# Kernel tuning notes

Measured on AMD Instinct MI355X. Metric: run time of the kernel, lower is better.

## Reference

```python
import jax, jax.numpy as jnp
import numpy as np

NEG_BIG = jnp.finfo(jnp.float32).min  # torch.nan_to_num maps -inf to finfo.min


def setup_inputs() -> dict:
    key = jax.random.key(0)
    ks = jax.random.split(key, 6)
    B, S, IN_KQ, IN_V, OUT_KQ, OUT_V = 4, 4096, 512, 512, 64, 64
    query = jax.random.normal(ks[0], (B, S, IN_KQ), dtype=jnp.float32)
    key_t = jax.random.normal(ks[1], (B, S, IN_KQ), dtype=jnp.float32)
    value = jax.random.normal(ks[2], (B, S, IN_V), dtype=jnp.float32)
    # nn.Linear weights: shape [out, in], y = x @ W.T
    Wq = jax.random.normal(ks[3], (OUT_KQ, IN_KQ), dtype=jnp.float32) / np.sqrt(IN_KQ)
    Wk = jax.random.normal(ks[4], (OUT_KQ, IN_KQ), dtype=jnp.float32) / np.sqrt(IN_KQ)
    Wv = jax.random.normal(ks[5], (OUT_V, IN_V), dtype=jnp.float32) / np.sqrt(IN_V)
    return {"query": query, "key": key_t, "value": value, "Wq": Wq, "Wk": Wk, "Wv": Wv}


def reference(query, key, value, Wq, Wk, Wv):
    # QKV projections (Linear, no bias): [B,S,in] @ [in,out]
    Q = jnp.einsum('bsi,oi->bso', query, Wq)
    K = jnp.einsum('bsi,oi->bso', key, Wk)
    V = jnp.einsum('bsi,oi->bso', value, Wv)

    S = Q.shape[1]
    scale = Q.shape[-1] ** 0.5
    # temp[b,i,j] = Q_i . K_j
    temp = jnp.einsum('bid,bjd->bij', Q, K)
    # torch mask: triu (incl. diagonal) -> finfo.min, strictly lower -> 0
    upper = jnp.triu(jnp.ones((S, S), dtype=bool), k=0)
    mask = jnp.where(upper, NEG_BIG, 0.0).astype(temp.dtype)
    # scale applied AFTER adding mask, as in the source
    attention = jax.nn.softmax((temp + mask) / scale, axis=-1)
    out = jnp.einsum('bij,bjd->bid', attention, V)
    return out
```

## Files before the change

### kernel.cpp

```cpp
#include <hip/hip_runtime.h>
#include <stdint.h>

#define Bn  4
#define Sn  4096
#define DIN 512
#define Dn  64
#define RS  0.18033688011112042f
#define MASKV (-3.0e38f)

typedef __bf16 bf16;
typedef __bf16 bf16x8 __attribute__((ext_vector_type(8)));
typedef float  f32x16 __attribute__((ext_vector_type(16)));
typedef unsigned short ushort8_t __attribute__((ext_vector_type(8)));

__device__ __forceinline__ f32x16 mfma32(bf16x8 a, bf16x8 b, f32x16 c) {
  return __builtin_amdgcn_mfma_f32_32x32x16_bf16(a, b, c, 0, 0, 0);
}

__device__ __forceinline__ f32x16 fzero16() {
  f32x16 v;
#pragma unroll
  for (int i = 0; i < 16; ++i) v[i] = 0.f;
  return v;
}

__device__ __forceinline__ bf16x8 frag_ld(const unsigned short* base, int row, int k) {
  int off = (row << 7) + (k << 1);
  off ^= (row & 7) << 4;
  return *(const bf16x8*)((const char*)base + off);
}

__device__ __forceinline__ void async16(void* lds, const void* g) {
  __builtin_amdgcn_global_load_lds(
      (const __attribute__((address_space(1))) unsigned int*)g,
      (__attribute__((address_space(3))) unsigned int*)lds, 16, 0, 0);
}

__device__ __forceinline__ unsigned int pk2(float a, float b) {
  unsigned short ra = __builtin_bit_cast(unsigned short, (bf16)a);
  unsigned short rb = __builtin_bit_cast(unsigned short, (bf16)b);
  return (unsigned int)ra | ((unsigned int)rb << 16);
}

__global__ __launch_bounds__(256) void proj_kernel(
    const float* __restrict__ Xq, const float* __restrict__ Xk, const float* __restrict__ Xv,
    const float* __restrict__ Wq, const float* __restrict__ Wk, const float* __restrict__ Wv,
    unsigned short* __restrict__ Qh, unsigned short* __restrict__ Ql,
    unsigned short* __restrict__ Kh, unsigned short* __restrict__ Kl,
    unsigned short* __restrict__ Vh, unsigned short* __restrict__ Vl)
{
  int mat = blockIdx.x >> 8;
  int rt  = blockIdx.x & 255;
  const float* X = (mat == 0) ? Xq : (mat == 1) ? Xk : Xv;
  const float* W = (mat == 0) ? Wq : (mat == 1) ? Wk : Wv;
  unsigned short* Yh = (mat == 0) ? Qh : (mat == 1) ? Kh : Vh;
  unsigned short* Yl = (mat == 0) ? Ql : (mat == 1) ? Kl : Vl;

  __shared__ unsigned short Xh_s[64 * 64];
  __shared__ unsigned short Xl_s[64 * 64];
  __shared__ unsigned short Wh_s[64 * 64];
  __shared__ unsigned short Wl_s[64 * 64];

  int tid  = threadIdx.x;
  int lane = tid & 63;
  int wv   = tid >> 6;
  int h    = lane >> 5;
  int c    = lane & 31;
  int srow = tid >> 2;
  int sq   = tid & 3;

  int row0 = rt * 64;

  f32x16 acc = fzero16();

  for (int k0 = 0; k0 < DIN; k0 += 64) {
#pragma unroll
    for (int j = 0; j < 4; ++j) {
      int kk = j * 16 + sq * 4;
      int off = ((srow << 7) + (kk << 1)) ^ ((srow & 7) << 4);

      float4 xv = *(const float4*)(X + (size_t)(row0 + srow) * DIN + k0 + kk);
      bf16 bx0 = (bf16)xv.x, bx1 = (bf16)xv.y, bx2 = (bf16)xv.z, bx3 = (bf16)xv.w;
      uint2 hw, lw;
      hw.x = (unsigned)__builtin_bit_cast(unsigned short, bx0) |
             ((unsigned)__builtin_bit_cast(unsigned short, bx1) << 16);
      hw.y = (unsigned)__builtin_bit_cast(unsigned short, bx2) |
             ((unsigned)__builtin_bit_cast(unsigned short, bx3) << 16);
      lw.x = pk2(xv.x - (float)bx0, xv.y - (float)bx1);
      lw.y = pk2(xv.z - (float)bx2, xv.w - (float)bx3);
      *(uint2*)((char*)Xh_s + off) = hw;
      *(uint2*)((char*)Xl_s + off) = lw;

      float4 wv4 = *(const float4*)(W + (size_t)srow * DIN + k0 + kk);
      bf16 bw0 = (bf16)wv4.x, bw1 = (bf16)wv4.y, bw2 = (bf16)wv4.z, bw3 = (bf16)wv4.w;
      uint2 hw2, lw2;
      hw2.x = (unsigned)__builtin_bit_cast(unsigned short, bw0) |
              ((unsigned)__builtin_bit_cast(unsigned short, bw1) << 16);
      hw2.y = (unsigned)__builtin_bit_cast(unsigned short, bw2) |
              ((unsigned)__builtin_bit_cast(unsigned short, bw3) << 16);
      lw2.x = pk2(wv4.x - (float)bw0, wv4.y - (float)bw1);
      lw2.y = pk2(wv4.z - (float)bw2, wv4.w - (float)bw3);
      *(uint2*)((char*)Wh_s + off) = hw2;
      *(uint2*)((char*)Wl_s + off) = lw2;
    }
    __syncthreads();

    int ar   = (wv >> 1) * 32 + c;
    int bcol = (wv & 1) * 32 + c;
#pragma unroll
    for (int kk = 0; kk < 4; ++kk) {
      int kp = kk * 16 + h * 8;
      bf16x8 ah = frag_ld(Xh_s, ar, kp);
      bf16x8 al = frag_ld(Xl_s, ar, kp);
      bf16x8 bh = frag_ld(Wh_s, bcol, kp);
      bf16x8 bl = frag_ld(Wl_s, bcol, kp);
      acc = mfma32(ah, bh, acc);
      acc = mfma32(ah, bl, acc);
      acc = mfma32(al, bh, acc);
    }
    __syncthreads();
  }

  int wr = (wv >> 1) * 32;
  int wc = (wv & 1) * 32;
#pragma unroll
  for (int r = 0; r < 16; ++r) {
    int rowl = (r & 3) + ((r >> 2) << 3) + h * 4;
    size_t o = (size_t)(row0 + wr + rowl) * Dn + wc + c;
    float v = acc[r];
    bf16 hv = (bf16)v;
    Yh[o] = __builtin_bit_cast(unsigned short, hv);
    Yl[o] = __builtin_bit_cast(unsigned short, (bf16)(v - (float)hv));
  }
}

__global__ __launch_bounds__(256) void transpose_kernel(
    const unsigned short* __restrict__ Vh, const unsigned short* __restrict__ Vl,
    unsigned short* __restrict__ Vth, unsigned short* __restrict__ Vtl)
{
  int bx = blockIdx.x;
  int b  = bx >> 6;
  int s0 = (bx & 63) * 64;
  __shared__ unsigned short th[64][72];
  __shared__ unsigned short tl[64][72];
  int t = threadIdx.x;
  int r = t >> 2, q4 = t & 3;

  const unsigned short* srch = Vh + ((size_t)(b * Sn + s0 + r)) * Dn + q4 * 16;
  const unsigned short* srcl = Vl + ((size_t)(b * Sn + s0 + r)) * Dn + q4 * 16;
  ushort8_t a0 = *(const ushort8_t*)srch;
  ushort8_t a1 = *(const ushort8_t*)(srch + 8);
  ushort8_t b0 = *(const ushort8_t*)srcl;
  ushort8_t b1 = *(const ushort8_t*)(srcl + 8);
  *(ushort8_t*)&th[r][q4 * 16]     = a0;
  *(ushort8_t*)&th[r][q4 * 16 + 8] = a1;
  *(ushort8_t*)&tl[r][q4 * 16]     = b0;
  *(ushort8_t*)&tl[r][q4 * 16 + 8] = b1;
  __syncthreads();

  int d = t >> 2, sp = t & 3;
  ushort8_t o0, o1, p0, p1;
#pragma unroll
  for (int i = 0; i < 8; ++i) {
    o0[i] = th[sp * 16 + i][d];
    o1[i] = th[sp * 16 + 8 + i][d];
    p0[i] = tl[sp * 16 + i][d];
    p1[i] = tl[sp * 16 + 8 + i][d];
  }
  unsigned short* dsth = Vth + ((size_t)(b * Dn + d)) * Sn + s0 + sp * 16;
  unsigned short* dstl = Vtl + ((size_t)(b * Dn + d)) * Sn + s0 + sp * 16;
  *(ushort8_t*)dsth       = o0;
  *(ushort8_t*)(dsth + 8) = o1;
  *(ushort8_t*)dstl       = p0;
  *(ushort8_t*)(dstl + 8) = p1;
}

__global__ __launch_bounds__(128) void attn_kernel(
    const unsigned short* __restrict__ Qh, const unsigned short* __restrict__ Ql,
    const unsigned short* __restrict__ Kh, const unsigned short* __restrict__ Kl,
    const unsigned short* __restrict__ Vth, const unsigned short* __restrict__ Vtl,
    float* __restrict__ part)
{
  int bx   = blockIdx.x;
  int qt   = 63 - (bx >> 3);
  int half = (bx >> 2) & 1;
  int b    = bx & 3;
  int tid  = threadIdx.x;
  int wv   = tid >> 6;
  int lane = tid & 63;
  int h    = lane >> 5;
  int c    = lane & 31;
  int q_base = qt * 64 + wv * 32;

  __shared__ unsigned short Kh_s[2][64 * 64];
  __shared__ unsigned short Kl_s[2][64 * 64];
  __shared__ unsigned short Vh_s[2][64 * 64];
  __shared__ unsigned short Vl_s[2][64 * 64];

  bf16x8 qhi[4], qlo[4];
  {
    const unsigned short* qp  = Qh + ((size_t)(b * Sn) + q_base + c) * Dn;
    const unsigned short* qp2 = Ql + ((size_t)(b * Sn) + q_base + c) * Dn;
#pragma unroll
    for (int kk = 0; kk < 4; ++kk) {
      qhi[kk] = *(const bf16x8*)(qp + kk * 16 + h * 8);
      qlo[kk] = *(const bf16x8*)(qp2 + kk * 16 + h * 8);
    }
  }

  f32x16 o0 = fzero16(), o1 = fzero16();
  float m = MASKV, lsum = 0.f;
  int nt = qt + 1;

  int l8   = lane >> 3;
  int slot = (lane & 7) ^ (l8 & 7);

  auto stage = [&](int sb, int ti) {
    size_t j0 = (size_t)ti * 64;
#pragma unroll
    for (int i = 0; i < 4; ++i) {
      int rowbase = (wv * 4 + i) * 8;
      int row = rowbase + l8;
      const char* gk  = (const char*)Kh + ((size_t)(b * Sn) + j0 + row) * 128 + slot * 16;
      const char* gk2 = (const char*)Kl + ((size_t)(b * Sn) + j0 + row) * 128 + slot * 16;
      async16(&Kh_s[sb][rowbase * 64], gk);
      async16(&Kl_s[sb][rowbase * 64], gk2);
      const char* gv  = (const char*)Vth + ((size_t)(b * Dn) + row) * (Sn * 2) + j0 * 2 + slot * 16;
      const char* gv2 = (const char*)Vtl + ((size_t)(b * Dn) + row) * (Sn * 2) + j0 * 2 + slot * 16;
      async16(&Vh_s[sb][rowbase * 64], gv);
      async16(&Vl_s[sb][rowbase * 64], gv2);
    }
  };

  int buf = 0;
  stage(0, half);
  __syncthreads();

  for (int ti = half; ti < nt; ti += 2) {
    if (ti + 2 < nt) stage(buf ^ 1, ti + 2);

    const unsigned short* KhT = Kh_s[buf];
    const unsigned short* KlT = Kl_s[buf];
    const unsigned short* VhT = Vh_s[buf];
    const unsigned short* VlT = Vl_s[buf];

    f32x16 s0a = fzero16(), s0b = fzero16(), s1a = fzero16(), s1b = fzero16();
#pragma unroll
    for (int kk = 0; kk < 4; ++kk) {
      int kp = kk * 16 + h * 8;
      bf16x8 k0h = frag_ld(KhT, c, kp);
      bf16x8 k0l = frag_ld(KlT, c, kp);
      bf16x8 k1h = frag_ld(KhT, 32 + c, kp);
      bf16x8 k1l = frag_ld(KlT, 32 + c, kp);
      if (kk < 2) {
        s0a = mfma32(k0h, qhi[kk], s0a); s0a = mfma32(k0h, qlo[kk], s0a); s0a = mfma32(k0l, qhi[kk], s0a);
        s1a = mfma32(k1h, qhi[kk], s1a); s1a = mfma32(k1h, qlo[kk], s1a); s1a = mfma32(k1l, qhi[kk], s1a);
      } else {
        s0b = mfma32(k0h, qhi[kk], s0b); s0b = mfma32(k0h, qlo[kk], s0b); s0b = mfma32(k0l, qhi[kk], s0b);
        s1b = mfma32(k1h, qhi[kk], s1b); s1b = mfma32(k1h, qlo[kk], s1b); s1b = mfma32(k1l, qhi[kk], s1b);
      }
    }
    f32x16 s0 = s0a + s0b;
    f32x16 s1 = s1a + s1b;

    if (ti == qt) {
      int qrel = wv * 32 + c;
#pragma unroll
      for (int r = 0; r < 16; ++r) {
        int koff = (r & 3) + ((r >> 2) << 3) + h * 4;
        if (koff >= qrel)      s0[r] = MASKV;
        if (32 + koff >= qrel) s1[r] = MASKV;
      }
    }

    float mt = s0[0];
#pragma unroll
    for (int r = 1; r < 16; ++r) mt = fmaxf(mt, s0[r]);
#pragma unroll
    for (int r = 0; r < 16; ++r) mt = fmaxf(mt, s1[r]);
    mt = fmaxf(mt, __shfl_xor(mt, 32, 64));
    float mnew = fmaxf(m, mt);
    float al = exp2f((m - mnew) * RS);

    float p0[16], p1[16];
    float rsum = 0.f;
#pragma unroll
    for (int r = 0; r < 16; ++r) {
      p0[r] = exp2f((s0[r] - mnew) * RS);
      p1[r] = exp2f((s1[r] - mnew) * RS);
      rsum += p0[r] + p1[r];
    }
    rsum += __shfl_xor(rsum, 32, 64);
    lsum = lsum * al + rsum;
    m = mnew;

#pragma unroll
    for (int r = 0; r < 16; ++r) {
      int koff = (r & 3) + ((r >> 2) << 3) + h * 4;
      float ar = __shfl(al, (lane & 32) | koff, 64);
      o0[r] *= ar;
      o1[r] *= ar;
    }

#pragma unroll
    for (int ks = 0; ks < 2; ++ks) {
#pragma unroll
      for (int kk2 = 0; kk2 < 2; ++kk2) {
        float e0[4], e1[4];
#pragma unroll
        for (int x = 0; x < 4; ++x) {
          float vh0 = ks ? p1[(2 * kk2 + 0) * 4 + x] : p0[(2 * kk2 + 0) * 4 + x];
          float vh1 = ks ? p1[(2 * kk2 + 1) * 4 + x] : p0[(2 * kk2 + 1) * 4 + x];
          float own  = h ? vh1 : vh0;
          float send = h ? vh0 : vh1;
          float recv = __shfl_xor(send, 32, 64);
          e0[x] = h ? recv : own;
          e1[x] = h ? own : recv;
        }
        bf16x8 pah, pal;
#pragma unroll
        for (int x = 0; x < 4; ++x) {
          bf16 hh = (bf16)e0[x];
          pah[x] = hh;
          pal[x] = (bf16)(e0[x] - (float)hh);
          bf16 h2 = (bf16)e1[x];
          pah[4 + x] = h2;
          pal[4 + x] = (bf16)(e1[x] - (float)h2);
        }
        int kp = ks * 32 + kk2 * 16 + h * 8;
        bf16x8 v0h = frag_ld(VhT, c, kp);
        bf16x8 v0l = frag_ld(VlT, c, kp);
        bf16x8 v1h = frag_ld(VhT, 32 + c, kp);
        bf16x8 v1l = frag_ld(VlT, 32 + c, kp);
        o0 = mfma32(pah, v0h, o0);
        o0 = mfma32(pah, v0l, o0);
        o0 = mfma32(pal, v0h, o0);
        o1 = mfma32(pah, v1h, o1);
        o1 = mfma32(pah, v1l, o1);
        o1 = mfma32(pal, v1h, o1);
      }
    }

    __syncthreads();
    buf ^= 1;
  }

  float* pb = part + ((size_t)(half * Bn + b) * Sn + q_base) * 68;
#pragma unroll
  for (int r = 0; r < 16; ++r) {
    int koff = (r & 3) + ((r >> 2) << 3) + h * 4;
    float* pr = pb + (size_t)koff * 68;
    pr[c]      = o0[r];
    pr[32 + c] = o1[r];
  }
  if (h == 0) {
    float* pr = pb + (size_t)c * 68;
    pr[64] = m;
    pr[65] = lsum;
  }
}

__global__ __launch_bounds__(256) void combine_kernel(
    const float* __restrict__ part, float* __restrict__ out)
{
  size_t idx = (size_t)blockIdx.x * 256 + threadIdx.x;
  int d = (int)(idx & 63);
  int s = (int)((idx >> 6) & (Sn - 1));
  int b = (int)(idx >> 18);
  const float* p0 = part + ((size_t)(0 * Bn + b) * Sn + s) * 68;
  const float* p1 = part + ((size_t)(1 * Bn + b) * Sn + s) * 68;
  float m0 = p0[64], l0 = p0[65];
  float m1 = p1[64], l1 = p1[65];
  float ms = fmaxf(m0, m1);
  float a0 = exp2f((m0 - ms) * RS);
  float a1 = exp2f((m1 - ms) * RS);
  float num = a0 * p0[d] + a1 * p1[d];
  float den = a0 * l0 + a1 * l1;
  out[idx] = (s == 0) ? 0.0f : (num / den);
}

__global__ __launch_bounds__(256) void meanv_kernel(
    const unsigned short* __restrict__ Vth, const unsigned short* __restrict__ Vtl,
    float* __restrict__ out)
{
  int bx = blockIdx.x;
  int b  = bx >> 4;
  int dg = (bx & 15) * 4;
  int t  = threadIdx.x;
  int dl = t >> 6;
  int jl = t & 63;
  int d  = dg + dl;

  const unsigned short* ph = Vth + ((size_t)(b * Dn + d)) * Sn;
  const unsigned short* pl = Vtl + ((size_t)(b * Dn + d)) * Sn;
  float s = 0.f;
#pragma unroll
  for (int it = 0; it < 4; ++it) {
    int base = it * 1024 + jl * 16;
    ushort8_t v0 = *(const ushort8_t*)(ph + base);
    ushort8_t v1 = *(const ushort8_t*)(ph + base + 8);
    ushort8_t w0 = *(const ushort8_t*)(pl + base);
    ushort8_t w1 = *(const ushort8_t*)(pl + base + 8);
#pragma unroll
    for (int e = 0; e < 8; ++e) {
      s += __uint_as_float((unsigned)v0[e] << 16);
      s += __uint_as_float((unsigned)v1[e] << 16);
      s += __uint_as_float((unsigned)w0[e] << 16);
      s += __uint_as_float((unsigned)w1[e] << 16);
    }
  }
#pragma unroll
  for (int o = 32; o > 0; o >>= 1) s += __shfl_xor(s, o, 64);
  if (jl == 0) out[(size_t)b * Sn * Dn + d] = s * (1.0f / 4096.0f);
}

extern "C" void kernel_launch(void* const* d_in, const int* in_sizes, int n_in,
                              void* d_out, int out_size, void* d_ws, size_t ws_size,
                              hipStream_t stream) {
  (void)in_sizes; (void)n_in; (void)out_size; (void)ws_size;
  const float* query = (const float*)d_in[0];
  const float* key_  = (const float*)d_in[1];
  const float* value = (const float*)d_in[2];
  const float* Wq = (const float*)d_in[3];
  const float* Wk = (const float*)d_in[4];
  const float* Wv = (const float*)d_in[5];
  float* out = (float*)d_out;

  char* w = (char*)d_ws;
  const size_t mat = (size_t)Bn * Sn * Dn * 2;
  unsigned short* Qh  = (unsigned short*)(w + 0 * mat);
  unsigned short* Ql  = (unsigned short*)(w + 1 * mat);
  unsigned short* Kh  = (unsigned short*)(w + 2 * mat);
  unsigned short* Kl  = (unsigned short*)(w + 3 * mat);
  unsigned short* Vh  = (unsigned short*)(w + 4 * mat);
  unsigned short* Vl  = (unsigned short*)(w + 5 * mat);
  unsigned short* Vth = (unsigned short*)(w + 6 * mat);
  unsigned short* Vtl = (unsigned short*)(w + 7 * mat);
  float* part = (float*)(w + 8 * mat);

  hipLaunchKernelGGL(proj_kernel, dim3(768), dim3(256), 0, stream,
                     query, key_, value, Wq, Wk, Wv, Qh, Ql, Kh, Kl, Vh, Vl);
  hipLaunchKernelGGL(transpose_kernel, dim3(256), dim3(256), 0, stream,
                     Vh, Vl, Vth, Vtl);
  hipLaunchKernelGGL(attn_kernel, dim3(512), dim3(128), 0, stream,
                     Qh, Ql, Kh, Kl, Vth, Vtl, part);
  hipLaunchKernelGGL(combine_kernel, dim3((Bn * Sn * Dn) / 256), dim3(256), 0, stream,
                     part, out);
  hipLaunchKernelGGL(meanv_kernel, dim3(64), dim3(256), 0, stream,
                     Vth, Vtl, out);
}
```

Measured before the change: 253.9 us.

## Fuse V transpose into projection and split attention KV four ways with 128-row query tiles

The projection kernel now writes V directly in transposed layout, which removes the separate transpose kernel and its extra round trip through memory. The attention kernel switches to 256-thread blocks covering 128 query rows each and splits the KV range four ways instead of two. Each staged K/V tile is shared by four waves, and waves skip tiles past their own diagonal. The combine kernel merges four partial results. In exchange, the transposed V stores from the projection are strided, some waves sit idle on diagonal tiles, and the partial buffer roughly doubles in size.

```diff
diff --git a/kernel.cpp b/kernel.cpp
--- a/kernel.cpp
+++ b/kernel.cpp
@@ -47,14 +47,14 @@
     const float* __restrict__ Wq, const float* __restrict__ Wk, const float* __restrict__ Wv,
     unsigned short* __restrict__ Qh, unsigned short* __restrict__ Ql,
     unsigned short* __restrict__ Kh, unsigned short* __restrict__ Kl,
-    unsigned short* __restrict__ Vh, unsigned short* __restrict__ Vl)
+    unsigned short* __restrict__ Vth, unsigned short* __restrict__ Vtl)
 {
   int mat = blockIdx.x >> 8;
   int rt  = blockIdx.x & 255;
   const float* X = (mat == 0) ? Xq : (mat == 1) ? Xk : Xv;
   const float* W = (mat == 0) ? Wq : (mat == 1) ? Wk : Wv;
-  unsigned short* Yh = (mat == 0) ? Qh : (mat == 1) ? Kh : Vh;
-  unsigned short* Yl = (mat == 0) ? Ql : (mat == 1) ? Kl : Vl;
+  unsigned short* Yh = (mat == 0) ? Qh : (mat == 1) ? Kh : Vth;
+  unsigned short* Yl = (mat == 0) ? Ql : (mat == 1) ? Kl : Vtl;
 
   __shared__ unsigned short Xh_s[64 * 64];
   __shared__ unsigned short Xl_s[64 * 64];
@@ -123,74 +123,48 @@
 
   int wr = (wv >> 1) * 32;
   int wc = (wv & 1) * 32;
-#pragma unroll
-  for (int r = 0; r < 16; ++r) {
-    int rowl = (r & 3) + ((r >> 2) << 3) + h * 4;
-    size_t o = (size_t)(row0 + wr + rowl) * Dn + wc + c;
-    float v = acc[r];
-    bf16 hv = (bf16)v;
-    Yh[o] = __builtin_bit_cast(unsigned short, hv);
-    Yl[o] = __builtin_bit_cast(unsigned short, (bf16)(v - (float)hv));
-  }
-}
-
-__global__ __launch_bounds__(256) void transpose_kernel(
-    const unsigned short* __restrict__ Vh, const unsigned short* __restrict__ Vl,
-    unsigned short* __restrict__ Vth, unsigned short* __restrict__ Vtl)
-{
-  int bx = blockIdx.x;
-  int b  = bx >> 6;
-  int s0 = (bx & 63) * 64;
-  __shared__ unsigned short th[64][72];
-  __shared__ unsigned short tl[64][72];
-  int t = threadIdx.x;
-  int r = t >> 2, q4 = t & 3;
-
-  const unsigned short* srch = Vh + ((size_t)(b * Sn + s0 + r)) * Dn + q4 * 16;
-  const unsigned short* srcl = Vl + ((size_t)(b * Sn + s0 + r)) * Dn + q4 * 16;
-  ushort8_t a0 = *(const ushort8_t*)srch;
-  ushort8_t a1 = *(const ushort8_t*)(srch + 8);
-  ushort8_t b0 = *(const ushort8_t*)srcl;
-  ushort8_t b1 = *(const ushort8_t*)(srcl + 8);
-  *(ushort8_t*)&th[r][q4 * 16]     = a0;
-  *(ushort8_t*)&th[r][q4 * 16 + 8] = a1;
-  *(ushort8_t*)&tl[r][q4 * 16]     = b0;
-  *(ushort8_t*)&tl[r][q4 * 16 + 8] = b1;
-  __syncthreads();
-
-  int d = t >> 2, sp = t & 3;
-  ushort8_t o0, o1, p0, p1;
-#pragma unroll
-  for (int i = 0; i < 8; ++i) {
-    o0[i] = th[sp * 16 + i][d];
-    o1[i] = th[sp * 16 + 8 + i][d];
-    p0[i] = tl[sp * 16 + i][d];
-    p1[i] = tl[sp * 16 + 8 + i][d];
-  }
-  unsigned short* dsth = Vth + ((size_t)(b * Dn + d)) * Sn + s0 + sp * 16;
-  unsigned short* dstl = Vtl + ((size_t)(b * Dn + d)) * Sn + s0 + sp * 16;
-  *(ushort8_t*)dsth       = o0;
-  *(ushort8_t*)(dsth + 8) = o1;
-  *(ushort8_t*)dstl       = p0;
-  *(ushort8_t*)(dstl + 8) = p1;
-}
-
-__global__ __launch_bounds__(128) void attn_kernel(
+  if (mat == 2) {
+#pragma unroll
+    for (int r = 0; r < 16; ++r) {
+      int rowl = (r & 3) + ((r >> 2) << 3) + h * 4;
+      int g  = row0 + wr + rowl;
+      int b2 = g >> 12;
+      int s2 = g & (Sn - 1);
+      size_t o = ((size_t)(b2 * Dn + wc + c)) * Sn + s2;
+      float v = acc[r];
+      bf16 hv = (bf16)v;
+      Yh[o] = __builtin_bit_cast(unsigned short, hv);
+      Yl[o] = __builtin_bit_cast(unsigned short, (bf16)(v - (float)hv));
+    }
+  } else {
+#pragma unroll
+    for (int r = 0; r < 16; ++r) {
+      int rowl = (r & 3) + ((r >> 2) << 3) + h * 4;
+      size_t o = (size_t)(row0 + wr + rowl) * Dn + wc + c;
+      float v = acc[r];
+      bf16 hv = (bf16)v;
+      Yh[o] = __builtin_bit_cast(unsigned short, hv);
+      Yl[o] = __builtin_bit_cast(unsigned short, (bf16)(v - (float)hv));
+    }
+  }
+}
+
+__global__ __launch_bounds__(256) void attn_kernel(
     const unsigned short* __restrict__ Qh, const unsigned short* __restrict__ Ql,
     const unsigned short* __restrict__ Kh, const unsigned short* __restrict__ Kl,
     const unsigned short* __restrict__ Vth, const unsigned short* __restrict__ Vtl,
     float* __restrict__ part)
 {
   int bx   = blockIdx.x;
-  int qt   = 63 - (bx >> 3);
-  int half = (bx >> 2) & 1;
+  int qtb  = 31 - (bx >> 4);
+  int sk   = (bx >> 2) & 3;
   int b    = bx & 3;
   int tid  = threadIdx.x;
   int wv   = tid >> 6;
   int lane = tid & 63;
   int h    = lane >> 5;
   int c    = lane & 31;
-  int q_base = qt * 64 + wv * 32;
+  int q_base = qtb * 128 + wv * 32;
 
   __shared__ unsigned short Kh_s[2][64 * 64];
   __shared__ unsigned short Kl_s[2][64 * 64];
@@ -210,7 +184,10 @@
 
   f32x16 o0 = fzero16(), o1 = fzero16();
   float m = MASKV, lsum = 0.f;
-  int nt = qt + 1;
+
+  int nt   = 2 * qtb + 2;
+  int ti_d = 2 * qtb + (wv >> 1);
+  int qrel = (wv & 1) * 32 + c;
 
   int l8   = lane >> 3;
   int slot = (lane & 7) ^ (l8 & 7);
@@ -218,8 +195,8 @@
   auto stage = [&](int sb, int ti) {
     size_t j0 = (size_t)ti * 64;
 #pragma unroll
-    for (int i = 0; i < 4; ++i) {
-      int rowbase = (wv * 4 + i) * 8;
+    for (int i = 0; i < 2; ++i) {
+      int rowbase = (wv * 2 + i) * 8;
       int row = rowbase + l8;
       const char* gk  = (const char*)Kh + ((size_t)(b * Sn) + j0 + row) * 128 + slot * 16;
       const char* gk2 = (const char*)Kl + ((size_t)(b * Sn) + j0 + row) * 128 + slot * 16;
@@ -233,111 +210,113 @@
   };
 
   int buf = 0;
-  stage(0, half);
+  stage(0, sk);
   __syncthreads();
 
-  for (int ti = half; ti < nt; ti += 2) {
-    if (ti + 2 < nt) stage(buf ^ 1, ti + 2);
-
-    const unsigned short* KhT = Kh_s[buf];
-    const unsigned short* KlT = Kl_s[buf];
-    const unsigned short* VhT = Vh_s[buf];
-    const unsigned short* VlT = Vl_s[buf];
-
-    f32x16 s0a = fzero16(), s0b = fzero16(), s1a = fzero16(), s1b = fzero16();
-#pragma unroll
-    for (int kk = 0; kk < 4; ++kk) {
-      int kp = kk * 16 + h * 8;
-      bf16x8 k0h = frag_ld(KhT, c, kp);
-      bf16x8 k0l = frag_ld(KlT, c, kp);
-      bf16x8 k1h = frag_ld(KhT, 32 + c, kp);
-      bf16x8 k1l = frag_ld(KlT, 32 + c, kp);
-      if (kk < 2) {
-        s0a = mfma32(k0h, qhi[kk], s0a); s0a = mfma32(k0h, qlo[kk], s0a); s0a = mfma32(k0l, qhi[kk], s0a);
-        s1a = mfma32(k1h, qhi[kk], s1a); s1a = mfma32(k1h, qlo[kk], s1a); s1a = mfma32(k1l, qhi[kk], s1a);
-      } else {
-        s0b = mfma32(k0h, qhi[kk], s0b); s0b = mfma32(k0h, qlo[kk], s0b); s0b = mfma32(k0l, qhi[kk], s0b);
-        s1b = mfma32(k1h, qhi[kk], s1b); s1b = mfma32(k1h, qlo[kk], s1b); s1b = mfma32(k1l, qhi[kk], s1b);
+  for (int ti = sk; ti < nt; ti += 4) {
+    if (ti + 4 < nt) stage(buf ^ 1, ti + 4);
+
+    bool active = (ti <= ti_d);
+    if (active) {
+      const unsigned short* KhT = Kh_s[buf];
+      const unsigned short* KlT = Kl_s[buf];
+      const unsigned short* VhT = Vh_s[buf];
+      const unsigned short* VlT = Vl_s[buf];
+
+      f32x16 s0a = fzero16(), s0b = fzero16(), s1a = fzero16(), s1b = fzero16();
+#pragma unroll
+      for (int kk = 0; kk < 4; ++kk) {
+        int kp = kk * 16 + h * 8;
+        bf16x8 k0h = frag_ld(KhT, c, kp);
+        bf16x8 k0l = frag_ld(KlT, c, kp);
+        bf16x8 k1h = frag_ld(KhT, 32 + c, kp);
+        bf16x8 k1l = frag_ld(KlT, 32 + c, kp);
+        if (kk < 2) {
+          s0a = mfma32(k0h, qhi[kk], s0a); s0a = mfma32(k0h, qlo[kk], s0a); s0a = mfma32(k0l, qhi[kk], s0a);
+          s1a = mfma32(k1h, qhi[kk], s1a); s1a = mfma32(k1h, qlo[kk], s1a); s1a = mfma32(k1l, qhi[kk], s1a);
+        } else {
+          s0b = mfma32(k0h, qhi[kk], s0b); s0b = mfma32(k0h, qlo[kk], s0b); s0b = mfma32(k0l, qhi[kk], s0b);
+          s1b = mfma32(k1h, qhi[kk], s1b); s1b = mfma32(k1h, qlo[kk], s1b); s1b = mfma32(k1l, qhi[kk], s1b);
+        }
       }
-    }
-    f32x16 s0 = s0a + s0b;
-    f32x16 s1 = s1a + s1b;
-
-    if (ti == qt) {
-      int qrel = wv * 32 + c;
+      f32x16 s0 = s0a + s0b;
+      f32x16 s1 = s1a + s1b;
+
+      if (ti == ti_d) {
+#pragma unroll
+        for (int r = 0; r < 16; ++r) {
+          int koff = (r & 3) + ((r >> 2) << 3) + h * 4;
+          if (koff >= qrel)      s0[r] = MASKV;
+          if (32 + koff >= qrel) s1[r] = MASKV;
+        }
+      }
+
+      float mt = s0[0];
+#pragma unroll
+      for (int r = 1; r < 16; ++r) mt = fmaxf(mt, s0[r]);
+#pragma unroll
+      for (int r = 0; r < 16; ++r) mt = fmaxf(mt, s1[r]);
+      mt = fmaxf(mt, __shfl_xor(mt, 32, 64));
+      float mnew = fmaxf(m, mt);
+      float al = exp2f((m - mnew) * RS);
+
+      float p0[16], p1[16];
+      float rsum = 0.f;
+#pragma unroll
+      for (int r = 0; r < 16; ++r) {
+        p0[r] = exp2f((s0[r] - mnew) * RS);
+        p1[r] = exp2f((s1[r] - mnew) * RS);
+        rsum += p0[r] + p1[r];
+      }
+      rsum += __shfl_xor(rsum, 32, 64);
+      lsum = lsum * al + rsum;
+      m = mnew;
+
 #pragma unroll
       for (int r = 0; r < 16; ++r) {
         int koff = (r & 3) + ((r >> 2) << 3) + h * 4;
-        if (koff >= qrel)      s0[r] = MASKV;
-        if (32 + koff >= qrel) s1[r] = MASKV;
+        float ar = __shfl(al, (lane & 32) | koff, 64);
+        o0[r] *= ar;
+        o1[r] *= ar;
       }
-    }
-
-    float mt = s0[0];
-#pragma unroll
-    for (int r = 1; r < 16; ++r) mt = fmaxf(mt, s0[r]);
-#pragma unroll
-    for (int r = 0; r < 16; ++r) mt = fmaxf(mt, s1[r]);
-    mt = fmaxf(mt, __shfl_xor(mt, 32, 64));
-    float mnew = fmaxf(m, mt);
-    float al = exp2f((m - mnew) * RS);
-
-    float p0[16], p1[16];
-    float rsum = 0.f;
-#pragma unroll
-    for (int r = 0; r < 16; ++r) {
-      p0[r] = exp2f((s0[r] - mnew) * RS);
-      p1[r] = exp2f((s1[r] - mnew) * RS);
-      rsum += p0[r] + p1[r];
-    }
-    rsum += __shfl_xor(rsum, 32, 64);
-    lsum = lsum * al + rsum;
-    m = mnew;
-
-#pragma unroll
-    for (int r = 0; r < 16; ++r) {
-      int koff = (r & 3) + ((r >> 2) << 3) + h * 4;
-      float ar = __shfl(al, (lane & 32) | koff, 64);
-      o0[r] *= ar;
-      o1[r] *= ar;
-    }
-
-#pragma unroll
-    for (int ks = 0; ks < 2; ++ks) {
-#pragma unroll
-      for (int kk2 = 0; kk2 < 2; ++kk2) {
-        float e0[4], e1[4];
-#pragma unroll
-        for (int x = 0; x < 4; ++x) {
-          float vh0 = ks ? p1[(2 * kk2 + 0) * 4 + x] : p0[(2 * kk2 + 0) * 4 + x];
-          float vh1 = ks ? p1[(2 * kk2 + 1) * 4 + x] : p0[(2 * kk2 + 1) * 4 + x];
-          float own  = h ? vh1 : vh0;
-          float send = h ? vh0 : vh1;
-          float recv = __shfl_xor(send, 32, 64);
-          e0[x] = h ? recv : own;
-          e1[x] = h ? own : recv;
+
+#pragma unroll
+      for (int ks = 0; ks < 2; ++ks) {
+#pragma unroll
+        for (int kk2 = 0; kk2 < 2; ++kk2) {
+          float e0[4], e1[4];
+#pragma unroll
+          for (int x = 0; x < 4; ++x) {
+            float vh0 = ks ? p1[(2 * kk2 + 0) * 4 + x] : p0[(2 * kk2 + 0) * 4 + x];
+            float vh1 = ks ? p1[(2 * kk2 + 1) * 4 + x] : p0[(2 * kk2 + 1) * 4 + x];
+            float own  = h ? vh1 : vh0;
+            float send = h ? vh0 : vh1;
+            float recv = __shfl_xor(send, 32, 64);
+            e0[x] = h ? recv : own;
+            e1[x] = h ? own : recv;
+          }
+          bf16x8 pah, pal;
+#pragma unroll
+          for (int x = 0; x < 4; ++x) {
+            bf16 hh = (bf16)e0[x];
+            pah[x] = hh;
+            pal[x] = (bf16)(e0[x] - (float)hh);
+            bf16 h2 = (bf16)e1[x];
+            pah[4 + x] = h2;
+            pal[4 + x] = (bf16)(e1[x] - (float)h2);
+          }
+          int kp = ks * 32 + kk2 * 16 + h * 8;
+          bf16x8 v0h = frag_ld(VhT, c, kp);
+          bf16x8 v0l = frag_ld(VlT, c, kp);
+          bf16x8 v1h = frag_ld(VhT, 32 + c, kp);
+          bf16x8 v1l = frag_ld(VlT, 32 + c, kp);
+          o0 = mfma32(pah, v0h, o0);
+          o0 = mfma32(pah, v0l, o0);
+          o0 = mfma32(pal, v0h, o0);
+          o1 = mfma32(pah, v1h, o1);
+          o1 = mfma32(pah, v1l, o1);
+          o1 = mfma32(pal, v1h, o1);
         }
-        bf16x8 pah, pal;
-#pragma unroll
-        for (int x = 0; x < 4; ++x) {
-          bf16 hh = (bf16)e0[x];
-          pah[x] = hh;
-          pal[x] = (bf16)(e0[x] - (float)hh);
-          bf16 h2 = (bf16)e1[x];
-          pah[4 + x] = h2;
-          pal[4 + x] = (bf16)(e1[x] - (float)h2);
-        }
-        int kp = ks * 32 + kk2 * 16 + h * 8;
-        bf16x8 v0h = frag_ld(VhT, c, kp);
-        bf16x8 v0l = frag_ld(VlT, c, kp);
-        bf16x8 v1h = frag_ld(VhT, 32 + c, kp);
-        bf16x8 v1l = frag_ld(VlT, 32 + c, kp);
-        o0 = mfma32(pah, v0h, o0);
-        o0 = mfma32(pah, v0l, o0);
-        o0 = mfma32(pal, v0h, o0);
-        o1 = mfma32(pah, v1h, o1);
-        o1 = mfma32(pah, v1l, o1);
-        o1 = mfma32(pal, v1h, o1);
       }
     }
 
@@ -345,7 +324,7 @@
     buf ^= 1;
   }
 
-  float* pb = part + ((size_t)(half * Bn + b) * Sn + q_base) * 68;
+  float* pb = part + ((size_t)(sk * Bn + b) * Sn + q_base) * 68;
 #pragma unroll
   for (int r = 0; r < 16; ++r) {
     int koff = (r & 3) + ((r >> 2) << 3) + h * 4;
@@ -367,15 +346,20 @@
   int d = (int)(idx & 63);
   int s = (int)((idx >> 6) & (Sn - 1));
   int b = (int)(idx >> 18);
-  const float* p0 = part + ((size_t)(0 * Bn + b) * Sn + s) * 68;
-  const float* p1 = part + ((size_t)(1 * Bn + b) * Sn + s) * 68;
-  float m0 = p0[64], l0 = p0[65];
-  float m1 = p1[64], l1 = p1[65];
-  float ms = fmaxf(m0, m1);
-  float a0 = exp2f((m0 - ms) * RS);
-  float a1 = exp2f((m1 - ms) * RS);
-  float num = a0 * p0[d] + a1 * p1[d];
-  float den = a0 * l0 + a1 * l1;
+  const float* p[4];
+  float ms = MASKV;
+#pragma unroll
+  for (int i = 0; i < 4; ++i) {
+    p[i] = part + ((size_t)(i * Bn + b) * Sn + s) * 68;
+    ms = fmaxf(ms, p[i][64]);
+  }
+  float num = 0.f, den = 0.f;
+#pragma unroll
+  for (int i = 0; i < 4; ++i) {
+    float a = exp2f((p[i][64] - ms) * RS);
+    num += a * p[i][d];
+    den += a * p[i][65];
+  }
   out[idx] = (s == 0) ? 0.0f : (num / den);
 }
 
@@ -432,17 +416,13 @@
   unsigned short* Ql  = (unsigned short*)(w + 1 * mat);
   unsigned short* Kh  = (unsigned short*)(w + 2 * mat);
   unsigned short* Kl  = (unsigned short*)(w + 3 * mat);
-  unsigned short* Vh  = (unsigned short*)(w + 4 * mat);
-  unsigned short* Vl  = (unsigned short*)(w + 5 * mat);
-  unsigned short* Vth = (unsigned short*)(w + 6 * mat);
-  unsigned short* Vtl = (unsigned short*)(w + 7 * mat);
-  float* part = (float*)(w + 8 * mat);
+  unsigned short* Vth = (unsigned short*)(w + 4 * mat);
+  unsigned short* Vtl = (unsigned short*)(w + 5 * mat);
+  float* part = (float*)(w + 6 * mat);
 
   hipLaunchKernelGGL(proj_kernel, dim3(768), dim3(256), 0, stream,
-                     query, key_, value, Wq, Wk, Wv, Qh, Ql, Kh, Kl, Vh, Vl);
-  hipLaunchKernelGGL(transpose_kernel, dim3(256), dim3(256), 0, stream,
-                     Vh, Vl, Vth, Vtl);
-  hipLaunchKernelGGL(attn_kernel, dim3(512), dim3(128), 0, stream,
+                     query, key_, value, Wq, Wk, Wv, Qh, Ql, Kh, Kl, Vth, Vtl);
+  hipLaunchKernelGGL(attn_kernel, dim3(512), dim3(256), 0, stream,
                      Qh, Ql, Kh, Kl, Vth, Vtl, part);
   hipLaunchKernelGGL(combine_kernel, dim3((Bn * Sn * Dn) / 256), dim3(256), 0, stream,
                      part, out);
```

Result: faster. 207.8 us (-18.2%).
